# Performance work log

Measured on AMD Instinct MI355X. Metric: run time of the kernel, lower is better.

## Reference

```python
import jax, jax.numpy as jnp
import numpy as np

H = 16
D_MODEL = 1024
D_HEAD = D_MODEL // H  # 64


def _xavier(key, shape):
    # xavier_uniform over last two dims (matches torch init on [h, in, out])
    fan_in, fan_out = shape[-2], shape[-1]
    limit = float(np.sqrt(6.0 / (fan_in + fan_out)))
    return jax.random.uniform(key, shape, jnp.float32, -limit, limit)


def setup_inputs() -> dict:
    key = jax.random.key(0)
    ks = jax.random.split(key, 7)
    B, S = 4, 2048
    x_q = jax.random.normal(ks[0], (B, S, D_MODEL), jnp.float32)
    x_k = jax.random.normal(ks[1], (B, S, D_MODEL), jnp.float32)
    x_v = jax.random.normal(ks[2], (B, S, D_MODEL), jnp.float32)
    W_Q = _xavier(ks[3], (H, D_MODEL, D_HEAD))
    W_K = _xavier(ks[4], (H, D_MODEL, D_HEAD))
    W_V = _xavier(ks[5], (H, D_MODEL, D_HEAD))
    # torch Linear weight: [out_features, in_features], y = x @ W^T
    lim = float(np.sqrt(6.0 / (2 * D_MODEL)))  # kaiming-uniform-ish default approximated by xavier for reproducibility
    W_O = jax.random.uniform(ks[6], (D_MODEL, D_MODEL), jnp.float32, -lim, lim)
    return {"x_q": x_q, "x_k": x_k, "x_v": x_v,
            "W_Q": W_Q, "W_K": W_K, "W_V": W_V, "W_O": W_O}


def reference(x_q, x_k, x_v, W_Q, W_K, W_V, W_O):
    d_scale = jnp.asarray(D_HEAD, jnp.float32) ** 0.25  # d_q == d_k == dim_q**(1/4)
    # per-head projections: [b,s,m] x [h,m,d] -> [b,h,s,d]
    Q = jnp.einsum('bsm,hmd->bhsd', x_q, W_Q)
    K = jnp.einsum('bsm,hmd->bhsd', x_k, W_K)
    V = jnp.einsum('bsm,hmd->bhsd', x_v, W_V)
    # column softmax over K^T: shape [b,h,d,s], softmax over dim=-2 (the d axis)
    Kt = jnp.swapaxes(K, -1, -2) / d_scale          # [b,h,d,s]
    Kt = jax.nn.softmax(Kt, axis=-2)
    A = jnp.einsum('bhds,bhse->bhde', Kt, V)        # KV precompute [b,h,d,d]
    Qs = jax.nn.softmax(Q / d_scale, axis=-1)       # row softmax over head dim
    Bt = jnp.einsum('bhsd,bhde->bhse', Qs, A)       # [b,h,s,d]
    b, h, s, d = Bt.shape
    # faithful to torch .view on contiguous [b,h,s,d] -> [b,s,h*d] (pure reshape, no transpose)
    Bt = Bt.reshape(b, s, h * d)
    return jnp.einsum('bsi,oi->bso', Bt, W_O)
```

## Files before the change

kernel.cpp:

```cpp
#include <hip/hip_runtime.h>
#include <cstdint>
#include <cstddef>

#define DMODEL 1024
#define HEADS  16
#define DHEAD  64
#define BATCH  4
#define SEQ    2048
#define ROWS   (BATCH * SEQ)
#define INV_DSCALE 0.3535533905932738f

typedef float  f32x4  __attribute__((ext_vector_type(4)));
typedef __bf16 bf16x8 __attribute__((ext_vector_type(8)));

__device__ __forceinline__ unsigned short f2bf(float x) {
    union { float f; unsigned u; } c; c.f = x;
    unsigned u = c.u;
    return (unsigned short)((u + 0x7fffu + ((u >> 16) & 1u)) >> 16);
}

__device__ __forceinline__ unsigned cvt_pk_bf16(float a, float b) {
#if __has_builtin(__builtin_amdgcn_cvt_pk_bf16_f32)
    typedef __bf16 bf16x2_t __attribute__((ext_vector_type(2)));
    union { bf16x2_t v; unsigned u; } c;
    c.v = __builtin_amdgcn_cvt_pk_bf16_f32(a, b);
    return c.u;
#else
    return (unsigned)f2bf(a) | ((unsigned)f2bf(b) << 16);
#endif
}

__device__ __forceinline__ void load_g2l16(const unsigned short* g, unsigned short* l) {
    __builtin_amdgcn_global_load_lds(
        (const __attribute__((address_space(1))) unsigned int*)g,
        (__attribute__((address_space(3))) unsigned int*)l,
        16 , 0 , 0 );
}

__global__ __launch_bounds__(256) void prep_w(const float* __restrict__ W0,
                                              const float* __restrict__ W1,
                                              const float* __restrict__ W2,
                                              const float* __restrict__ Wo,
                                              const float* __restrict__ Xq,
                                              const float* __restrict__ Xk,
                                              const float* __restrict__ Xv,
                                              unsigned short* __restrict__ T0,
                                              unsigned short* __restrict__ T1,
                                              unsigned short* __restrict__ T2,
                                              unsigned short* __restrict__ To,
                                              unsigned short* __restrict__ Xb) {
    __shared__ float tile[64][68];
    int blk = blockIdx.x;
    int t = threadIdx.x;
    if (blk < 768) {
        int w = blk >> 8, h = (blk >> 4) & 15, mb = blk & 15;
        const float* W = w == 0 ? W0 : (w == 1 ? W1 : W2);
        unsigned short* T = w == 0 ? T0 : (w == 1 ? T1 : T2);
        #pragma unroll
        for (int i = 0; i < 4; ++i) {
            int f = t + 256 * i;
            int m = f >> 4, dg = (f & 15) * 4;
            *(float4*)&tile[m][dg] = *(const float4*)&W[((size_t)(h * 16 + mb) * 64 + m) * 64 + dg];
        }
        __syncthreads();
        #pragma unroll
        for (int i = 0; i < 2; ++i) {
            int f = t + 256 * i;
            int d = f >> 3, mg = f & 7;
            ushort4 a, b;
            a.x = f2bf(tile[mg * 8 + 0][d]); a.y = f2bf(tile[mg * 8 + 1][d]);
            a.z = f2bf(tile[mg * 8 + 2][d]); a.w = f2bf(tile[mg * 8 + 3][d]);
            b.x = f2bf(tile[mg * 8 + 4][d]); b.y = f2bf(tile[mg * 8 + 5][d]);
            b.z = f2bf(tile[mg * 8 + 6][d]); b.w = f2bf(tile[mg * 8 + 7][d]);
            unsigned short* dst = T + (size_t)(h * 64 + d) * DMODEL + mb * 64 + mg * 8;
            *(ushort4*)dst = a; *(ushort4*)(dst + 4) = b;
        }
    } else if (blk < 1024) {
        int wb = blk - 768;
        #pragma unroll
        for (int u = 0; u < 4; ++u) {
            int i = wb * 1024 + u * 256 + t;
            float4 v = ((const float4*)Wo)[i];
            ushort4 o;
            o.x = f2bf(v.x); o.y = f2bf(v.y); o.z = f2bf(v.z); o.w = f2bf(v.w);
            ((ushort4*)To)[i] = o;
        }
    } else {
        int bb = blk - 1024;
        int w = bb >> 10;
        int chunk = bb & 1023;
        const float* X = w == 0 ? Xq : (w == 1 ? Xk : Xv);
        unsigned short* D = Xb + (size_t)w * ROWS * DMODEL;
        #pragma unroll
        for (int u = 0; u < 4; ++u) {
            size_t g = (size_t)chunk * 1024 + u * 256 + t;
            const float4* src = (const float4*)X + g * 2;
            float4 a = src[0], bv = src[1];
            uint4 pk;
            pk.x = cvt_pk_bf16(a.x, a.y);
            pk.y = cvt_pk_bf16(a.z, a.w);
            pk.z = cvt_pk_bf16(bv.x, bv.y);
            pk.w = cvt_pk_bf16(bv.z, bv.w);
            ((uint4*)D)[g] = pk;
        }
    }
}

__device__ __forceinline__ void gemm_tile(const unsigned short* __restrict__ Ap,
                                          const unsigned short* __restrict__ Bp,
                                          int K, int bm0, int bn0,
                                          unsigned short* smem, f32x4 acc[4][4]) {
    unsigned short* ldsA = smem;
    unsigned short* ldsB = smem + 8192;

    const int t    = threadIdx.x;
    const int lane = t & 63;
    const int wave = t >> 6;
    const int wm   = (wave & 1) * 64;
    const int wn   = (wave >> 1) * 64;
    const int fr   = lane & 15;
    const int quad = lane >> 4;

    unsigned offA[4], offB[4];
    #pragma unroll
    for (int i = 0; i < 4; ++i) {
        int f = t + 256 * i, row = f >> 3, kg = (f & 7) ^ (row & 7);
        offA[i] = (unsigned)(bm0 + row) * K + kg * 8;
        offB[i] = (unsigned)(bn0 + row) * K + kg * 8;
    }

    for (int k0 = 0; k0 < K; k0 += 64) {
        #pragma unroll
        for (int i = 0; i < 4; ++i)
            load_g2l16(Ap + offA[i] + k0, &ldsA[(t + 256 * i) * 8]);
        #pragma unroll
        for (int i = 0; i < 4; ++i)
            load_g2l16(Bp + offB[i] + k0, &ldsB[(t + 256 * i) * 8]);
        asm volatile("s_waitcnt vmcnt(0)" ::: "memory");
        __syncthreads();

        bf16x8 af[4][2], bfr[4][2];
        #pragma unroll
        for (int i = 0; i < 4; ++i) {
            int row = wm + i * 16 + fr;
            #pragma unroll
            for (int kh = 0; kh < 2; ++kh) {
                int s = (kh * 4 + quad) ^ (row & 7);
                af[i][kh] = *reinterpret_cast<const bf16x8*>(&ldsA[row * 64 + s * 8]);
            }
        }
        #pragma unroll
        for (int j = 0; j < 4; ++j) {
            int row = wn + j * 16 + fr;
            #pragma unroll
            for (int kh = 0; kh < 2; ++kh) {
                int s = (kh * 4 + quad) ^ (row & 7);
                bfr[j][kh] = *reinterpret_cast<const bf16x8*>(&ldsB[row * 64 + s * 8]);
            }
        }
        #pragma unroll
        for (int kh = 0; kh < 2; ++kh)
            #pragma unroll
            for (int i = 0; i < 4; ++i)
                #pragma unroll
                for (int j = 0; j < 4; ++j)
                    acc[i][j] = __builtin_amdgcn_mfma_f32_16x16x32_bf16(af[i][kh], bfr[j][kh], acc[i][j], 0, 0, 0);

        __syncthreads();
    }
}

__device__ __forceinline__ void softmax4(float v[4]) {
    #pragma unroll
    for (int j = 0; j < 4; ++j) v[j] *= INV_DSCALE;
    float m = fmaxf(fmaxf(v[0], v[1]), fmaxf(v[2], v[3]));
    #pragma unroll
    for (int off = 8; off; off >>= 1) m = fmaxf(m, __shfl_xor(m, off, 16));
    float s = 0.f;
    #pragma unroll
    for (int j = 0; j < 4; ++j) { v[j] = __expf(v[j] - m); s += v[j]; }
    #pragma unroll
    for (int off = 8; off; off >>= 1) s += __shfl_xor(s, off, 16);
    float inv = 1.0f / s;
    #pragma unroll
    for (int j = 0; j < 4; ++j) v[j] *= inv;
}

__device__ __forceinline__ void decode_blk(int flat, int& bm0, int& bn0) {
    int xcd = flat & 7, idx = flat >> 3;
    bm0 = (xcd * 8 + (idx >> 3)) * 128;
    bn0 = (idx & 7) * 128;
}

__global__ __launch_bounds__(256, 2) void proj_kv(const unsigned short* __restrict__ Xb,
                                                  const unsigned short* __restrict__ wk,
                                                  const unsigned short* __restrict__ wv,
                                                  unsigned short* __restrict__ Kt,
                                                  unsigned short* __restrict__ Vt) {
    __shared__ unsigned short smem[17408];
    int z = blockIdx.y + 1;
    const unsigned short* A = Xb + (size_t)z * ROWS * DMODEL;
    const unsigned short* B = (z == 1) ? wk : wv;
    int bm0, bn0;
    decode_blk(blockIdx.x, bm0, bn0);

    f32x4 acc[4][4] = {};
    gemm_tile(A, B, DMODEL, bm0, bn0, smem, acc);

    const int t    = threadIdx.x;
    const int lane = t & 63;
    const int wave = t >> 6;
    const int wm   = (wave & 1) * 64;
    const int wn   = (wave >> 1) * 64;
    const int fr   = lane & 15;
    const int quad = lane >> 4;
    bool do_sm = (z == 1);

    unsigned short* Ct = smem;
    #pragma unroll
    for (int i = 0; i < 4; ++i)
        #pragma unroll
        for (int r = 0; r < 4; ++r) {
            float v[4];
            #pragma unroll
            for (int j = 0; j < 4; ++j) v[j] = acc[i][j][r];
            if (do_sm) softmax4(v);
            int rr = wm + i * 16 + quad * 4 + r;
            #pragma unroll
            for (int j = 0; j < 4; ++j) {
                int cc = wn + j * 16 + fr;
                Ct[cc * 136 + rr] = f2bf(v[j]);
            }
        }
    __syncthreads();
    unsigned short* T = (z == 1) ? Kt : Vt;
    int c = t >> 1, sh = (t & 1) * 64;
    int col = bn0 + c, h = col >> 6, d = col & 63;
    int b = bm0 >> 11, s0 = bm0 & 2047;
    unsigned short* dst = T + (((size_t)(b * 16 + h) * 64 + d) << 11) + s0 + sh;
    const unsigned short* src = &smem[c * 136 + sh];
    #pragma unroll
    for (int k = 0; k < 8; ++k)
        *(uint4*)(dst + k * 8) = *(const uint4*)(src + k * 8);
}

__global__ __launch_bounds__(256, 2) void proj_q(const unsigned short* __restrict__ Xb,
                                                 const unsigned short* __restrict__ wq,
                                                 const unsigned short* __restrict__ At,
                                                 unsigned short* __restrict__ R) {
    __shared__ unsigned short smem[24576];
    int bm0, bn0;
    decode_blk(blockIdx.x, bm0, bn0);

    f32x4 acc[4][4] = {};
    gemm_tile(Xb, wq, DMODEL, bm0, bn0, smem, acc);

    const int t = threadIdx.x, lane = t & 63, wave = t >> 6;
    const int wm = (wave & 1) * 64, wn = (wave >> 1) * 64;
    const int fr = lane & 15, quad = lane >> 4;
    const int b = bm0 >> 11, s0 = bm0 & 2047;
    const int h0 = bn0 >> 6;
    const int bh_base = b * 16 + h0;

    unsigned short* Qs = smem;
    unsigned short* ldsAt = smem + 16384;

    #pragma unroll
    for (int i = 0; i < 4; ++i) {
        int f = t + 256 * i;
        int hd = f >> 9, row = (f >> 3) & 63, kg = (f & 7) ^ (row & 7);
        load_g2l16(At + (size_t)(bh_base + hd) * 4096 + row * 64 + kg * 8,
                   &ldsAt[f * 8]);
    }

    #pragma unroll
    for (int i = 0; i < 4; ++i)
        #pragma unroll
        for (int r = 0; r < 4; ++r) {
            float v[4];
            #pragma unroll
            for (int j = 0; j < 4; ++j) v[j] = acc[i][j][r];
            softmax4(v);
            int row = wm + i * 16 + quad * 4 + r;
            #pragma unroll
            for (int j = 0; j < 4; ++j) {
                int c = wn + j * 16 + fr;
                int cs = (c & 0x47) | (((((c >> 3) & 7) ^ (row & 7))) << 3);
                Qs[row * 128 + cs] = f2bf(v[j]);
            }
        }
    asm volatile("s_waitcnt vmcnt(0)" ::: "memory");
    __syncthreads();

    const int hw = wn >> 6;
    f32x4 racc[4][4] = {};
    #pragma unroll
    for (int kh = 0; kh < 2; ++kh) {
        bf16x8 aq[4], bt[4];
        #pragma unroll
        for (int i = 0; i < 4; ++i) {
            int row = wm + i * 16 + fr;
            int s = (kh * 4 + quad) ^ (row & 7);
            aq[i] = *reinterpret_cast<const bf16x8*>(&Qs[row * 128 + wn + s * 8]);
        }
        #pragma unroll
        for (int j = 0; j < 4; ++j) {
            int e = j * 16 + fr;
            int s = (kh * 4 + quad) ^ (e & 7);
            bt[j] = *reinterpret_cast<const bf16x8*>(&ldsAt[(hw << 12) + e * 64 + s * 8]);
        }
        #pragma unroll
        for (int i = 0; i < 4; ++i)
            #pragma unroll
            for (int j = 0; j < 4; ++j)
                racc[i][j] = __builtin_amdgcn_mfma_f32_16x16x32_bf16(aq[i], bt[j], racc[i][j], 0, 0, 0);
    }

    size_t bh = (size_t)(bh_base + hw);
    #pragma unroll
    for (int i = 0; i < 4; ++i)
        #pragma unroll
        for (int r = 0; r < 4; ++r) {
            int rr = wm + i * 16 + quad * 4 + r;
            size_t base = (bh << 17) + (size_t)(s0 + rr) * 64;
            #pragma unroll
            for (int j = 0; j < 4; ++j)
                R[base + j * 16 + fr] = f2bf(racc[i][j][r]);
        }
}

__global__ __launch_bounds__(256, 2) void gemm_out(const unsigned short* __restrict__ R,
                                                   const unsigned short* __restrict__ Wo,
                                                   float* __restrict__ out) {
    __shared__ unsigned short smem[16384];
    int bm0, bn0;
    decode_blk(blockIdx.x, bm0, bn0);
    f32x4 acc[4][4] = {};
    gemm_tile(R, Wo, DMODEL, bm0, bn0, smem, acc);

    const int t = threadIdx.x, lane = t & 63, wave = t >> 6;
    const int wm = (wave & 1) * 64, wn = (wave >> 1) * 64;
    const int fr = lane & 15, quad = lane >> 4;
    #pragma unroll
    for (int i = 0; i < 4; ++i)
        #pragma unroll
        for (int r = 0; r < 4; ++r) {
            int rr = bm0 + wm + i * 16 + quad * 4 + r;
            size_t base = (size_t)rr * DMODEL + bn0 + wn + fr;
            #pragma unroll
            for (int j = 0; j < 4; ++j) out[base + j * 16] = acc[i][j][r];
        }
}

__global__ __launch_bounds__(256) void kv_mfma(const unsigned short* __restrict__ Vt,
                                               const unsigned short* __restrict__ Kt,
                                               float* __restrict__ P) {
    __shared__ unsigned short ldsV[64 * 64];
    __shared__ unsigned short ldsK[64 * 64];
    int bh = blockIdx.x >> 3, chunk = blockIdx.x & 7;
    int t = threadIdx.x, lane = t & 63, wave = t >> 6;
    int fr = lane & 15, quad = lane >> 4;

    unsigned offV[2], offK[2];
    #pragma unroll
    for (int i = 0; i < 2; ++i) {
        int f = t + 256 * i, row = f >> 3, kg = (f & 7) ^ (row & 7);
        unsigned o = ((unsigned)(bh * 64 + row) << 11) + chunk * 256 + kg * 8;
        offV[i] = o; offK[i] = o;
    }

    f32x4 acc[4] = {};
    for (int k0 = 0; k0 < 256; k0 += 64) {
        #pragma unroll
        for (int i = 0; i < 2; ++i)
            load_g2l16(Vt + offV[i] + k0, &ldsV[(t + 256 * i) * 8]);
        #pragma unroll
        for (int i = 0; i < 2; ++i)
            load_g2l16(Kt + offK[i] + k0, &ldsK[(t + 256 * i) * 8]);
        asm volatile("s_waitcnt vmcnt(0)" ::: "memory");
        __syncthreads();

        #pragma unroll
        for (int kh = 0; kh < 2; ++kh) {
            int rowA = wave * 16 + fr;
            int sA = (kh * 4 + quad) ^ (rowA & 7);
            bf16x8 av = *reinterpret_cast<const bf16x8*>(&ldsV[rowA * 64 + sA * 8]);
            #pragma unroll
            for (int j = 0; j < 4; ++j) {
                int rowB = j * 16 + fr;
                int sB = (kh * 4 + quad) ^ (rowB & 7);
                bf16x8 bv = *reinterpret_cast<const bf16x8*>(&ldsK[rowB * 64 + sB * 8]);
                acc[j] = __builtin_amdgcn_mfma_f32_16x16x32_bf16(av, bv, acc[j], 0, 0, 0);
            }
        }
        __syncthreads();
    }
    float* Pp = P + ((size_t)chunk * 64 + bh) * 4096;
    #pragma unroll
    for (int j = 0; j < 4; ++j)
        #pragma unroll
        for (int r = 0; r < 4; ++r)
            Pp[(wave * 16 + quad * 4 + r) * 64 + j * 16 + fr] = acc[j][r];
}

__global__ __launch_bounds__(256) void reduce_A(const float* __restrict__ P,
                                                unsigned short* __restrict__ At) {
    int idx = blockIdx.x * 256 + threadIdx.x;
    float s = 0.f;
    #pragma unroll
    for (int c = 0; c < 8; ++c) s += P[(size_t)c * (64 * 4096) + idx];
    At[idx] = f2bf(s);
}

extern "C" void kernel_launch(void* const* d_in, const int* in_sizes, int n_in,
                              void* d_out, int out_size, void* d_ws, size_t ws_size,
                              hipStream_t stream) {
    const float* xq = (const float*)d_in[0];
    const float* xk = (const float*)d_in[1];
    const float* xv = (const float*)d_in[2];
    const float* Wq = (const float*)d_in[3];
    const float* Wk = (const float*)d_in[4];
    const float* Wv = (const float*)d_in[5];
    const float* Wo = (const float*)d_in[6];
    float* out = (float*)d_out;
    char* ws = (char*)d_ws;

    const size_t MB = 1ull << 20;
    unsigned short* wq_t = (unsigned short*)(ws + 0 * MB);
    unsigned short* wk_t = (unsigned short*)(ws + 2 * MB);
    unsigned short* wv_t = (unsigned short*)(ws + 4 * MB);
    unsigned short* wo_b = (unsigned short*)(ws + 6 * MB);
    unsigned short* Xb   = (unsigned short*)(ws + 8 * MB);
    unsigned short* Kt   = (unsigned short*)(ws + 56 * MB);
    unsigned short* Vt   = (unsigned short*)(ws + 72 * MB);
    unsigned short* At   = (unsigned short*)(ws + 88 * MB);
    float* P            = (float*)(ws + 24 * MB);
    unsigned short* R   = (unsigned short*)(ws + 40 * MB);

    prep_w<<<4096, 256, 0, stream>>>(Wq, Wk, Wv, Wo, xq, xk, xv,
                                     wq_t, wk_t, wv_t, wo_b, Xb);

    proj_kv<<<dim3(512, 2), 256, 0, stream>>>(Xb, wk_t, wv_t, Kt, Vt);

    kv_mfma<<<BATCH * HEADS * 8, 256, 0, stream>>>(Vt, Kt, P);
    reduce_A<<<1024, 256, 0, stream>>>(P, At);

    proj_q<<<512, 256, 0, stream>>>(Xb, wq_t, At, R);

    gemm_out<<<512, 256, 0, stream>>>(R, wo_b, out);
}
```

Before: 255.9 us.

## Fuse fp32-to-bf16 activation conversion into projection GEMM tile loads

Drops the separate pass that converted x_q, x_k and x_v to bf16 in workspace. The projection GEMMs now stream fp32 activations straight into a larger swizzled LDS tile and convert to bf16 while building MFMA fragments. This removes a full read-write pass over the activations. In exchange it doubles A-tile LDS footprint and global bytes per tile, and adds conversion work in the inner loop.

```diff
diff --git a/kernel.cpp b/kernel.cpp
--- a/kernel.cpp
+++ b/kernel.cpp
@@ -37,18 +37,21 @@
         16 , 0 , 0 );
 }
 
+__device__ __forceinline__ void load_g2l16f(const float* g, float* l) {
+    __builtin_amdgcn_global_load_lds(
+        (const __attribute__((address_space(1))) unsigned int*)g,
+        (__attribute__((address_space(3))) unsigned int*)l,
+        16 , 0 , 0 );
+}
+
 __global__ __launch_bounds__(256) void prep_w(const float* __restrict__ W0,
                                               const float* __restrict__ W1,
                                               const float* __restrict__ W2,
                                               const float* __restrict__ Wo,
-                                              const float* __restrict__ Xq,
-                                              const float* __restrict__ Xk,
-                                              const float* __restrict__ Xv,
                                               unsigned short* __restrict__ T0,
                                               unsigned short* __restrict__ T1,
                                               unsigned short* __restrict__ T2,
-                                              unsigned short* __restrict__ To,
-                                              unsigned short* __restrict__ Xb) {
+                                              unsigned short* __restrict__ To) {
     __shared__ float tile[64][68];
     int blk = blockIdx.x;
     int t = threadIdx.x;
@@ -75,7 +78,7 @@
             unsigned short* dst = T + (size_t)(h * 64 + d) * DMODEL + mb * 64 + mg * 8;
             *(ushort4*)dst = a; *(ushort4*)(dst + 4) = b;
         }
-    } else if (blk < 1024) {
+    } else {
         int wb = blk - 768;
         #pragma unroll
         for (int u = 0; u < 4; ++u) {
@@ -85,34 +88,15 @@
             o.x = f2bf(v.x); o.y = f2bf(v.y); o.z = f2bf(v.z); o.w = f2bf(v.w);
             ((ushort4*)To)[i] = o;
         }
-    } else {
-        int bb = blk - 1024;
-        int w = bb >> 10;
-        int chunk = bb & 1023;
-        const float* X = w == 0 ? Xq : (w == 1 ? Xk : Xv);
-        unsigned short* D = Xb + (size_t)w * ROWS * DMODEL;
-        #pragma unroll
-        for (int u = 0; u < 4; ++u) {
-            size_t g = (size_t)chunk * 1024 + u * 256 + t;
-            const float4* src = (const float4*)X + g * 2;
-            float4 a = src[0], bv = src[1];
-            uint4 pk;
-            pk.x = cvt_pk_bf16(a.x, a.y);
-            pk.y = cvt_pk_bf16(a.z, a.w);
-            pk.z = cvt_pk_bf16(bv.x, bv.y);
-            pk.w = cvt_pk_bf16(bv.z, bv.w);
-            ((uint4*)D)[g] = pk;
-        }
-    }
-}
-
-__device__ __forceinline__ void gemm_tile(const unsigned short* __restrict__ Ap,
+    }
+}
+
+template <bool AF32>
+__device__ __forceinline__ void gemm_tile(const void* __restrict__ Av,
                                           const unsigned short* __restrict__ Bp,
                                           int K, int bm0, int bn0,
                                           unsigned short* smem, f32x4 acc[4][4]) {
-    unsigned short* ldsA = smem;
-    unsigned short* ldsB = smem + 8192;
-
+    unsigned short* ldsB = smem + (AF32 ? 16384 : 8192);
     const int t    = threadIdx.x;
     const int lane = t & 63;
     const int wave = t >> 6;
@@ -121,18 +105,40 @@
     const int fr   = lane & 15;
     const int quad = lane >> 4;
 
-    unsigned offA[4], offB[4];
+    const float*          A32  = (const float*)Av;
+    const unsigned short* A16  = (const unsigned short*)Av;
+    float*                ldsAf = (float*)smem;
+    unsigned short*       ldsAh = smem;
+
+    constexpr int NA = AF32 ? 8 : 4;
+    unsigned offA[NA], offB[4];
+    #pragma unroll
+    for (int i = 0; i < NA; ++i) {
+        int f = t + 256 * i;
+        if (AF32) {
+            int row = f >> 4, sg = (f & 15) ^ (row & 15);
+            offA[i] = (unsigned)(bm0 + row) * K + sg * 4;
+        } else {
+            int row = f >> 3, kg = (f & 7) ^ (row & 7);
+            offA[i] = (unsigned)(bm0 + row) * K + kg * 8;
+        }
+    }
     #pragma unroll
     for (int i = 0; i < 4; ++i) {
         int f = t + 256 * i, row = f >> 3, kg = (f & 7) ^ (row & 7);
-        offA[i] = (unsigned)(bm0 + row) * K + kg * 8;
         offB[i] = (unsigned)(bn0 + row) * K + kg * 8;
     }
 
     for (int k0 = 0; k0 < K; k0 += 64) {
-        #pragma unroll
-        for (int i = 0; i < 4; ++i)
-            load_g2l16(Ap + offA[i] + k0, &ldsA[(t + 256 * i) * 8]);
+        if (AF32) {
+            #pragma unroll
+            for (int i = 0; i < 8; ++i)
+                load_g2l16f(A32 + offA[i] + k0, ldsAf + (t + 256 * i) * 4);
+        } else {
+            #pragma unroll
+            for (int i = 0; i < 4; ++i)
+                load_g2l16(A16 + offA[i] + k0, &ldsAh[(t + 256 * i) * 8]);
+        }
         #pragma unroll
         for (int i = 0; i < 4; ++i)
             load_g2l16(Bp + offB[i] + k0, &ldsB[(t + 256 * i) * 8]);
@@ -145,8 +151,21 @@
             int row = wm + i * 16 + fr;
             #pragma unroll
             for (int kh = 0; kh < 2; ++kh) {
-                int s = (kh * 4 + quad) ^ (row & 7);
-                af[i][kh] = *reinterpret_cast<const bf16x8*>(&ldsA[row * 64 + s * 8]);
+                if (AF32) {
+                    int g = 2 * (kh * 4 + quad), r15 = row & 15;
+                    const float* base = ldsAf + row * 64;
+                    float4 lo = *(const float4*)(base + ((g ^ r15) << 2));
+                    float4 hi = *(const float4*)(base + (((g + 1) ^ r15) << 2));
+                    union { uint4 u; bf16x8 v; } cv;
+                    cv.u.x = cvt_pk_bf16(lo.x, lo.y);
+                    cv.u.y = cvt_pk_bf16(lo.z, lo.w);
+                    cv.u.z = cvt_pk_bf16(hi.x, hi.y);
+                    cv.u.w = cvt_pk_bf16(hi.z, hi.w);
+                    af[i][kh] = cv.v;
+                } else {
+                    int s = (kh * 4 + quad) ^ (row & 7);
+                    af[i][kh] = *reinterpret_cast<const bf16x8*>(&ldsAh[row * 64 + s * 8]);
+                }
             }
         }
         #pragma unroll
@@ -192,20 +211,21 @@
     bn0 = (idx & 7) * 128;
 }
 
-__global__ __launch_bounds__(256, 2) void proj_kv(const unsigned short* __restrict__ Xb,
+__global__ __launch_bounds__(256, 2) void proj_kv(const float* __restrict__ xk,
+                                                  const float* __restrict__ xv,
                                                   const unsigned short* __restrict__ wk,
                                                   const unsigned short* __restrict__ wv,
                                                   unsigned short* __restrict__ Kt,
                                                   unsigned short* __restrict__ Vt) {
-    __shared__ unsigned short smem[17408];
-    int z = blockIdx.y + 1;
-    const unsigned short* A = Xb + (size_t)z * ROWS * DMODEL;
-    const unsigned short* B = (z == 1) ? wk : wv;
+    __shared__ unsigned short smem[24576];
+    int zk = blockIdx.y;
+    const float* A = zk == 0 ? xk : xv;
+    const unsigned short* B = zk == 0 ? wk : wv;
     int bm0, bn0;
     decode_blk(blockIdx.x, bm0, bn0);
 
     f32x4 acc[4][4] = {};
-    gemm_tile(A, B, DMODEL, bm0, bn0, smem, acc);
+    gemm_tile<true>(A, B, DMODEL, bm0, bn0, smem, acc);
 
     const int t    = threadIdx.x;
     const int lane = t & 63;
@@ -214,7 +234,7 @@
     const int wn   = (wave >> 1) * 64;
     const int fr   = lane & 15;
     const int quad = lane >> 4;
-    bool do_sm = (z == 1);
+    bool do_sm = (zk == 0);
 
     unsigned short* Ct = smem;
     #pragma unroll
@@ -233,7 +253,7 @@
             }
         }
     __syncthreads();
-    unsigned short* T = (z == 1) ? Kt : Vt;
+    unsigned short* T = (zk == 0) ? Kt : Vt;
     int c = t >> 1, sh = (t & 1) * 64;
     int col = bn0 + c, h = col >> 6, d = col & 63;
     int b = bm0 >> 11, s0 = bm0 & 2047;
@@ -244,16 +264,16 @@
         *(uint4*)(dst + k * 8) = *(const uint4*)(src + k * 8);
 }
 
-__global__ __launch_bounds__(256, 2) void proj_q(const unsigned short* __restrict__ Xb,
+__global__ __launch_bounds__(256, 2) void proj_q(const float* __restrict__ xq,
                                                  const unsigned short* __restrict__ wq,
                                                  const unsigned short* __restrict__ At,
                                                  unsigned short* __restrict__ R) {
-    __shared__ unsigned short smem[24576];
+    __shared__ unsigned short smem[32768];
     int bm0, bn0;
     decode_blk(blockIdx.x, bm0, bn0);
 
     f32x4 acc[4][4] = {};
-    gemm_tile(Xb, wq, DMODEL, bm0, bn0, smem, acc);
+    gemm_tile<true>(xq, wq, DMODEL, bm0, bn0, smem, acc);
 
     const int t = threadIdx.x, lane = t & 63, wave = t >> 6;
     const int wm = (wave & 1) * 64, wn = (wave >> 1) * 64;
@@ -263,7 +283,7 @@
     const int bh_base = b * 16 + h0;
 
     unsigned short* Qs = smem;
-    unsigned short* ldsAt = smem + 16384;
+    unsigned short* ldsAt = smem + 24576;
 
     #pragma unroll
     for (int i = 0; i < 4; ++i) {
@@ -336,7 +356,7 @@
     int bm0, bn0;
     decode_blk(blockIdx.x, bm0, bn0);
     f32x4 acc[4][4] = {};
-    gemm_tile(R, Wo, DMODEL, bm0, bn0, smem, acc);
+    gemm_tile<false>(R, Wo, DMODEL, bm0, bn0, smem, acc);
 
     const int t = threadIdx.x, lane = t & 63, wave = t >> 6;
     const int wm = (wave & 1) * 64, wn = (wave >> 1) * 64;
@@ -430,22 +450,20 @@
     unsigned short* wk_t = (unsigned short*)(ws + 2 * MB);
     unsigned short* wv_t = (unsigned short*)(ws + 4 * MB);
     unsigned short* wo_b = (unsigned short*)(ws + 6 * MB);
-    unsigned short* Xb   = (unsigned short*)(ws + 8 * MB);
-    unsigned short* Kt   = (unsigned short*)(ws + 56 * MB);
-    unsigned short* Vt   = (unsigned short*)(ws + 72 * MB);
-    unsigned short* At   = (unsigned short*)(ws + 88 * MB);
-    float* P            = (float*)(ws + 24 * MB);
-    unsigned short* R   = (unsigned short*)(ws + 40 * MB);
-
-    prep_w<<<4096, 256, 0, stream>>>(Wq, Wk, Wv, Wo, xq, xk, xv,
-                                     wq_t, wk_t, wv_t, wo_b, Xb);
-
-    proj_kv<<<dim3(512, 2), 256, 0, stream>>>(Xb, wk_t, wv_t, Kt, Vt);
+    unsigned short* Kt   = (unsigned short*)(ws + 8 * MB);
+    unsigned short* Vt   = (unsigned short*)(ws + 24 * MB);
+    unsigned short* At   = (unsigned short*)(ws + 40 * MB);
+    unsigned short* R    = (unsigned short*)(ws + 41 * MB);
+    float* P             = (float*)(ws + 57 * MB);
+
+    prep_w<<<1024, 256, 0, stream>>>(Wq, Wk, Wv, Wo, wq_t, wk_t, wv_t, wo_b);
+
+    proj_kv<<<dim3(512, 2), 256, 0, stream>>>(xk, xv, wk_t, wv_t, Kt, Vt);
 
     kv_mfma<<<BATCH * HEADS * 8, 256, 0, stream>>>(Vt, Kt, P);
     reduce_A<<<1024, 256, 0, stream>>>(P, At);
 
-    proj_q<<<512, 256, 0, stream>>>(Xb, wq_t, At, R);
+    proj_q<<<512, 256, 0, stream>>>(xq, wq_t, At, R);
 
     gemm_out<<<512, 256, 0, stream>>>(R, wo_b, out);
 }
```

New measurement: 293.0 us. 1.15x slower.

## Fuse split-K reduction into kv_mfma and move Q cast into proj_kv

Applied to the files above, without the earlier changes.

The separate reduce_A kernel is removed. The last-arriving chunk block per head, detected with an atomic counter that prep_w zeroes, now sums the partial P buffers and writes the bf16 A matrix. The x_q fp32-to-bf16 conversion moves from prep_w into extra blocks of proj_kv, so it runs alongside the K/V projection GEMM tail. This saves one kernel launch and shortens prep_w, at the cost of threadfence/atomic overhead and a serialized reduction in a few blocks.

```diff
diff --git a/kernel.cpp b/kernel.cpp
--- a/kernel.cpp
+++ b/kernel.cpp
@@ -41,14 +41,14 @@
                                               const float* __restrict__ W1,
                                               const float* __restrict__ W2,
                                               const float* __restrict__ Wo,
-                                              const float* __restrict__ Xq,
                                               const float* __restrict__ Xk,
                                               const float* __restrict__ Xv,
                                               unsigned short* __restrict__ T0,
                                               unsigned short* __restrict__ T1,
                                               unsigned short* __restrict__ T2,
                                               unsigned short* __restrict__ To,
-                                              unsigned short* __restrict__ Xb) {
+                                              unsigned short* __restrict__ Xb,
+                                              unsigned int* __restrict__ cnt) {
     __shared__ float tile[64][68];
     int blk = blockIdx.x;
     int t = threadIdx.x;
@@ -76,6 +76,7 @@
             *(ushort4*)dst = a; *(ushort4*)(dst + 4) = b;
         }
     } else if (blk < 1024) {
+        if (blk == 768 && t < 64) cnt[t] = 0;
         int wb = blk - 768;
         #pragma unroll
         for (int u = 0; u < 4; ++u) {
@@ -87,9 +88,9 @@
         }
     } else {
         int bb = blk - 1024;
-        int w = bb >> 10;
+        int w = 1 + (bb >> 10);
         int chunk = bb & 1023;
-        const float* X = w == 0 ? Xq : (w == 1 ? Xk : Xv);
+        const float* X = (w == 1) ? Xk : Xv;
         unsigned short* D = Xb + (size_t)w * ROWS * DMODEL;
         #pragma unroll
         for (int u = 0; u < 4; ++u) {
@@ -192,29 +193,49 @@
     bn0 = (idx & 7) * 128;
 }
 
-__global__ __launch_bounds__(256, 2) void proj_kv(const unsigned short* __restrict__ Xb,
+__global__ __launch_bounds__(256, 2) void proj_kv(const float* __restrict__ xq,
+                                                  const unsigned short* __restrict__ Xb,
                                                   const unsigned short* __restrict__ wk,
                                                   const unsigned short* __restrict__ wv,
                                                   unsigned short* __restrict__ Kt,
-                                                  unsigned short* __restrict__ Vt) {
+                                                  unsigned short* __restrict__ Vt,
+                                                  unsigned short* __restrict__ Xb0) {
     __shared__ unsigned short smem[17408];
-    int z = blockIdx.y + 1;
-    const unsigned short* A = Xb + (size_t)z * ROWS * DMODEL;
-    const unsigned short* B = (z == 1) ? wk : wv;
+    int id = blockIdx.x;
+    int t = threadIdx.x;
+    if (id >= 1024) {
+        int chunk = id - 1024;
+        #pragma unroll
+        for (int u = 0; u < 4; ++u) {
+            size_t g = (size_t)chunk * 1024 + u * 256 + t;
+            const float4* src = (const float4*)xq + g * 2;
+            float4 a = src[0], bv = src[1];
+            uint4 pk;
+            pk.x = cvt_pk_bf16(a.x, a.y);
+            pk.y = cvt_pk_bf16(a.z, a.w);
+            pk.z = cvt_pk_bf16(bv.x, bv.y);
+            pk.w = cvt_pk_bf16(bv.z, bv.w);
+            ((uint4*)Xb0)[g] = pk;
+        }
+        return;
+    }
+
+    int zk = id >> 9;
     int bm0, bn0;
-    decode_blk(blockIdx.x, bm0, bn0);
+    decode_blk(id & 511, bm0, bn0);
+    const unsigned short* A = Xb + (size_t)(zk + 1) * ROWS * DMODEL;
+    const unsigned short* B = (zk == 0) ? wk : wv;
 
     f32x4 acc[4][4] = {};
     gemm_tile(A, B, DMODEL, bm0, bn0, smem, acc);
 
-    const int t    = threadIdx.x;
     const int lane = t & 63;
     const int wave = t >> 6;
     const int wm   = (wave & 1) * 64;
     const int wn   = (wave >> 1) * 64;
     const int fr   = lane & 15;
     const int quad = lane >> 4;
-    bool do_sm = (z == 1);
+    bool do_sm = (zk == 0);
 
     unsigned short* Ct = smem;
     #pragma unroll
@@ -233,7 +254,7 @@
             }
         }
     __syncthreads();
-    unsigned short* T = (z == 1) ? Kt : Vt;
+    unsigned short* T = (zk == 0) ? Kt : Vt;
     int c = t >> 1, sh = (t & 1) * 64;
     int col = bn0 + c, h = col >> 6, d = col & 63;
     int b = bm0 >> 11, s0 = bm0 & 2047;
@@ -242,6 +263,73 @@
     #pragma unroll
     for (int k = 0; k < 8; ++k)
         *(uint4*)(dst + k * 8) = *(const uint4*)(src + k * 8);
+}
+
+__global__ __launch_bounds__(256) void kv_mfma(const unsigned short* __restrict__ Vt,
+                                               const unsigned short* __restrict__ Kt,
+                                               float* __restrict__ P,
+                                               unsigned short* __restrict__ At,
+                                               unsigned int* __restrict__ cnt) {
+    __shared__ unsigned short ldsV[64 * 64];
+    __shared__ unsigned short ldsK[64 * 64];
+    int bh = blockIdx.x >> 3, chunk = blockIdx.x & 7;
+    int t = threadIdx.x, lane = t & 63, wave = t >> 6;
+    int fr = lane & 15, quad = lane >> 4;
+
+    unsigned offVK[2];
+    #pragma unroll
+    for (int i = 0; i < 2; ++i) {
+        int f = t + 256 * i, row = f >> 3, kg = (f & 7) ^ (row & 7);
+        offVK[i] = ((unsigned)(bh * 64 + row) << 11) + chunk * 256 + kg * 8;
+    }
+
+    f32x4 acc[4] = {};
+    for (int k0 = 0; k0 < 256; k0 += 64) {
+        #pragma unroll
+        for (int i = 0; i < 2; ++i)
+            load_g2l16(Vt + offVK[i] + k0, &ldsV[(t + 256 * i) * 8]);
+        #pragma unroll
+        for (int i = 0; i < 2; ++i)
+            load_g2l16(Kt + offVK[i] + k0, &ldsK[(t + 256 * i) * 8]);
+        asm volatile("s_waitcnt vmcnt(0)" ::: "memory");
+        __syncthreads();
+
+        #pragma unroll
+        for (int kh = 0; kh < 2; ++kh) {
+            int rowA = wave * 16 + fr;
+            int sA = (kh * 4 + quad) ^ (rowA & 7);
+            bf16x8 av = *reinterpret_cast<const bf16x8*>(&ldsV[rowA * 64 + sA * 8]);
+            #pragma unroll
+            for (int j = 0; j < 4; ++j) {
+                int rowB = j * 16 + fr;
+                int sB = (kh * 4 + quad) ^ (rowB & 7);
+                bf16x8 bv = *reinterpret_cast<const bf16x8*>(&ldsK[rowB * 64 + sB * 8]);
+                acc[j] = __builtin_amdgcn_mfma_f32_16x16x32_bf16(av, bv, acc[j], 0, 0, 0);
+            }
+        }
+        __syncthreads();
+    }
+    float* Pp = P + ((size_t)chunk * 64 + bh) * 4096;
+    #pragma unroll
+    for (int j = 0; j < 4; ++j)
+        #pragma unroll
+        for (int r = 0; r < 4; ++r)
+            Pp[(wave * 16 + quad * 4 + r) * 64 + j * 16 + fr] = acc[j][r];
+
+    __threadfence();
+    __shared__ int last;
+    if (t == 0) last = (atomicAdd(&cnt[bh], 1u) == 7u);
+    __syncthreads();
+    if (last) {
+        const volatile float* Pv = P;
+        for (int idx = t; idx < 4096; idx += 256) {
+            float s = 0.f;
+            #pragma unroll
+            for (int c = 0; c < 8; ++c)
+                s += Pv[((size_t)c * 64 + bh) * 4096 + idx];
+            At[(size_t)bh * 4096 + idx] = f2bf(s);
+        }
+    }
 }
 
 __global__ __launch_bounds__(256, 2) void proj_q(const unsigned short* __restrict__ Xb,
@@ -350,66 +438,6 @@
             #pragma unroll
             for (int j = 0; j < 4; ++j) out[base + j * 16] = acc[i][j][r];
         }
-}
-
-__global__ __launch_bounds__(256) void kv_mfma(const unsigned short* __restrict__ Vt,
-                                               const unsigned short* __restrict__ Kt,
-                                               float* __restrict__ P) {
-    __shared__ unsigned short ldsV[64 * 64];
-    __shared__ unsigned short ldsK[64 * 64];
-    int bh = blockIdx.x >> 3, chunk = blockIdx.x & 7;
-    int t = threadIdx.x, lane = t & 63, wave = t >> 6;
-    int fr = lane & 15, quad = lane >> 4;
-
-    unsigned offV[2], offK[2];
-    #pragma unroll
-    for (int i = 0; i < 2; ++i) {
-        int f = t + 256 * i, row = f >> 3, kg = (f & 7) ^ (row & 7);
-        unsigned o = ((unsigned)(bh * 64 + row) << 11) + chunk * 256 + kg * 8;
-        offV[i] = o; offK[i] = o;
-    }
-
-    f32x4 acc[4] = {};
-    for (int k0 = 0; k0 < 256; k0 += 64) {
-        #pragma unroll
-        for (int i = 0; i < 2; ++i)
-            load_g2l16(Vt + offV[i] + k0, &ldsV[(t + 256 * i) * 8]);
-        #pragma unroll
-        for (int i = 0; i < 2; ++i)
-            load_g2l16(Kt + offK[i] + k0, &ldsK[(t + 256 * i) * 8]);
-        asm volatile("s_waitcnt vmcnt(0)" ::: "memory");
-        __syncthreads();
-
-        #pragma unroll
-        for (int kh = 0; kh < 2; ++kh) {
-            int rowA = wave * 16 + fr;
-            int sA = (kh * 4 + quad) ^ (rowA & 7);
-            bf16x8 av = *reinterpret_cast<const bf16x8*>(&ldsV[rowA * 64 + sA * 8]);
-            #pragma unroll
-            for (int j = 0; j < 4; ++j) {
-                int rowB = j * 16 + fr;
-                int sB = (kh * 4 + quad) ^ (rowB & 7);
-                bf16x8 bv = *reinterpret_cast<const bf16x8*>(&ldsK[rowB * 64 + sB * 8]);
-                acc[j] = __builtin_amdgcn_mfma_f32_16x16x32_bf16(av, bv, acc[j], 0, 0, 0);
-            }
-        }
-        __syncthreads();
-    }
-    float* Pp = P + ((size_t)chunk * 64 + bh) * 4096;
-    #pragma unroll
-    for (int j = 0; j < 4; ++j)
-        #pragma unroll
-        for (int r = 0; r < 4; ++r)
-            Pp[(wave * 16 + quad * 4 + r) * 64 + j * 16 + fr] = acc[j][r];
-}
-
-__global__ __launch_bounds__(256) void reduce_A(const float* __restrict__ P,
-                                                unsigned short* __restrict__ At) {
-    int idx = blockIdx.x * 256 + threadIdx.x;
-    float s = 0.f;
-    #pragma unroll
-    for (int c = 0; c < 8; ++c) s += P[(size_t)c * (64 * 4096) + idx];
-    At[idx] = f2bf(s);
 }
 
 extern "C" void kernel_launch(void* const* d_in, const int* in_sizes, int n_in,
@@ -434,16 +462,16 @@
     unsigned short* Kt   = (unsigned short*)(ws + 56 * MB);
     unsigned short* Vt   = (unsigned short*)(ws + 72 * MB);
     unsigned short* At   = (unsigned short*)(ws + 88 * MB);
+    unsigned int*  cnt   = (unsigned int*)(ws + 89 * MB);
     float* P            = (float*)(ws + 24 * MB);
     unsigned short* R   = (unsigned short*)(ws + 40 * MB);
 
-    prep_w<<<4096, 256, 0, stream>>>(Wq, Wk, Wv, Wo, xq, xk, xv,
-                                     wq_t, wk_t, wv_t, wo_b, Xb);
-
-    proj_kv<<<dim3(512, 2), 256, 0, stream>>>(Xb, wk_t, wv_t, Kt, Vt);
-
-    kv_mfma<<<BATCH * HEADS * 8, 256, 0, stream>>>(Vt, Kt, P);
-    reduce_A<<<1024, 256, 0, stream>>>(P, At);
+    prep_w<<<3072, 256, 0, stream>>>(Wq, Wk, Wv, Wo, xk, xv,
+                                     wq_t, wk_t, wv_t, wo_b, Xb, cnt);
+
+    proj_kv<<<2048, 256, 0, stream>>>(xq, Xb, wk_t, wv_t, Kt, Vt, Xb);
+
+    kv_mfma<<<BATCH * HEADS * 8, 256, 0, stream>>>(Vt, Kt, P, At, cnt);
 
     proj_q<<<512, 256, 0, stream>>>(Xb, wq_t, At, R);
 
```

Result: slower. 348.6 us (+36.2%).
